# Kernel optimization log

Measured on AMD Instinct MI355X. Metric: run time of the kernel, lower is better.

The kernel has to match this reference:

```python
import jax, jax.numpy as jnp
import numpy as np

D_MODEL, D_STATE, D_CONV, D_INNER = 1024, 16, 4, 2048
B, S = 1, 2048
EPS = 1e-5


def setup_inputs() -> dict:
    key = jax.random.key(0)
    ks = jax.random.split(key, 8)
    sc = 0.02
    return {
        "x": jax.random.normal(ks[0], (B, S, D_MODEL), jnp.float32),
        "ln_g": jnp.ones((D_MODEL,), jnp.float32),
        "ln_b": jnp.zeros((D_MODEL,), jnp.float32),
        "in_w": jax.random.normal(ks[1], (2 * D_INNER, D_MODEL), jnp.float32) * sc,
        "conv_w": jax.random.normal(ks[2], (D_INNER, 1, D_CONV), jnp.float32) * sc,  # depthwise OIH
        "conv_b": jax.random.normal(ks[3], (D_INNER,), jnp.float32) * sc,
        "xproj_w": jax.random.normal(ks[4], (2 * D_STATE + 1, D_INNER), jnp.float32) * sc,
        "dt_w": jax.random.normal(ks[5], (D_INNER, 1), jnp.float32) * sc,
        "dt_b": jax.random.normal(ks[6], (D_INNER,), jnp.float32) * sc,
        "A_log": jnp.log(jnp.arange(1, D_STATE + 1, dtype=jnp.float32)),
        "D": jnp.ones((D_INNER,), jnp.float32),
        "out_w": jax.random.normal(ks[7], (D_MODEL, D_INNER), jnp.float32) * sc,
    }


def reference(x, ln_g, ln_b, in_w, conv_w, conv_b, xproj_w, dt_w, dt_b, A_log, D, out_w):
    b, s, _ = x.shape
    d_inner = D.shape[0]
    d_state = A_log.shape[0]
    d_conv = conv_w.shape[-1]
    residual = x

    # LayerNorm
    mu = jnp.mean(x, axis=-1, keepdims=True)
    var = jnp.mean(jnp.square(x - mu), axis=-1, keepdims=True)
    xn = (x - mu) * jax.lax.rsqrt(var + EPS) * ln_g + ln_b

    # in_proj, split into x and gate z
    xz = jnp.einsum('bsd,ed->bse', xn, in_w)  # [B,S,2*d_inner]
    xi, z = jnp.split(xz, 2, axis=-1)

    # causal depthwise conv1d (torch pads d_conv-1 both sides then crops to seq_len)
    xc = jnp.transpose(xi, (0, 2, 1))  # [B,C,S]
    xc = jnp.pad(xc, ((0, 0), (0, 0), (d_conv - 1, 0)))
    xc = jax.lax.conv_general_dilated(
        xc, conv_w, window_strides=(1,), padding='VALID',
        dimension_numbers=('NCH', 'OIH', 'NCH'), feature_group_count=d_inner)
    xc = xc + conv_b[None, :, None]
    xs = jax.nn.silu(jnp.transpose(xc, (0, 2, 1)))  # [B,S,d_inner]

    # SSM projections
    xp = jnp.einsum('bsd,ed->bse', xs, xproj_w)  # [B,S,2*d_state+1]
    delta = jax.nn.softplus(xp[..., :1] * dt_w[:, 0] + dt_b)  # [B,S,d_inner]
    Bm = xp[..., 1:1 + d_state]  # [B,S,N]
    Cm = xp[..., 1 + d_state:]   # [B,S,N]
    A = -jnp.exp(A_log)          # [N]

    dA = jnp.exp(delta[..., None] * A)                      # [B,S,d_inner,N]
    dBx = delta[..., None] * Bm[:, :, None, :] * xs[..., None]  # [B,S,d_inner,N]

    def step(h, inp):
        dA_t, dBx_t, C_t = inp
        h = dA_t * h + dBx_t                     # [B,d_inner,N]
        y_t = jnp.einsum('bdn,bn->bd', h, C_t)   # [B,d_inner]
        return h, y_t

    h0 = jnp.zeros((b, d_inner, d_state), x.dtype)
    _, ys = jax.lax.scan(step, h0, (jnp.moveaxis(dA, 1, 0),
                                    jnp.moveaxis(dBx, 1, 0),
                                    jnp.moveaxis(Cm, 1, 0)))
    y = jnp.moveaxis(ys, 0, 1) + xs * D  # [B,S,d_inner]

    y = y * jax.nn.silu(z)
    out = jnp.einsum('bse,de->bsd', y, out_w)
    return out + residual
```

## Files before the change

### kernel.cpp

```cpp
#include <hip/hip_runtime.h>
#include <cstdint>
#include <cstddef>

#define D_MODEL 1024
#define D_STATE 16
#define D_CONV  4
#define D_INNER 2048
#define SEQ     2048
#define NCHUNK  128
#define CLEN    16
#define NGRP    8
#define GCH     16
#define LN_EPS  1e-5f

typedef unsigned short ushort_t;
typedef __attribute__((ext_vector_type(8))) short short8;
typedef __attribute__((ext_vector_type(4))) float f32x4;

__device__ __forceinline__ ushort_t f2bf(float x) {
  union { float f; uint32_t u; } v; v.f = x;
  uint32_t r = (v.u + 0x7fffu + ((v.u >> 16) & 1u)) >> 16;
  return (ushort_t)r;
}
__device__ __forceinline__ float bf2f(ushort_t u) {
  union { uint32_t x; float f; } v; v.x = ((uint32_t)u) << 16; return v.f;
}

__device__ __forceinline__ void async16(void* lds, const void* g) {
  __builtin_amdgcn_global_load_lds(
      (const __attribute__((address_space(1))) unsigned int*)g,
      (__attribute__((address_space(3))) unsigned int*)lds, 16, 0, 0);
}

__device__ __forceinline__ float softplus_f(float x) {
  if (x > 20.f) return x;
  if (x < -20.f) return __expf(x);
  return __logf(1.f + __expf(x));
}

__device__ __forceinline__ void dapow(float g1, float* da) {
  float g2 = g1 * g1, g4 = g2 * g2, g8 = g4 * g4;
  #pragma unroll
  for (int n = 0; n < 16; n++) {
    int e = n + 1;
    float v = (e & 1) ? g1 : 1.f;
    if (e & 2) v *= g2;
    if (e & 4) v *= g4;
    if (e & 8) v *= g8;
    da[n] = v;
  }
}

__global__ __launch_bounds__(256) void prep_kernel(const float* __restrict__ x,
                                                   const float* __restrict__ g,
                                                   const float* __restrict__ b,
                                                   const float* __restrict__ inw,
                                                   const float* __restrict__ outw,
                                                   const float* __restrict__ xpw,
                                                   ushort_t* __restrict__ xn_bf,
                                                   ushort_t* __restrict__ inw_bf,
                                                   ushort_t* __restrict__ outw_bf,
                                                   ushort_t* __restrict__ xpw_bf) {
  int blk = blockIdx.x;
  if (blk < SEQ) {
    int row = blk;
    const float4* xr = (const float4*)(x + (size_t)row * D_MODEL);
    float4 v = xr[threadIdx.x];
    float s  = v.x + v.y + v.z + v.w;
    float ss = v.x * v.x + v.y * v.y + v.z * v.z + v.w * v.w;
    #pragma unroll
    for (int o = 32; o; o >>= 1) { s += __shfl_down(s, o); ss += __shfl_down(ss, o); }
    __shared__ float sbuf[8], ssbuf[8];
    int wid = threadIdx.x >> 6, lane = threadIdx.x & 63;
    if (lane == 0) { sbuf[wid] = s; ssbuf[wid] = ss; }
    __syncthreads();
    if (threadIdx.x == 0) {
      float t = 0.f, t2 = 0.f;
      for (int i = 0; i < 4; i++) { t += sbuf[i]; t2 += ssbuf[i]; }
      float mu = t / D_MODEL;
      sbuf[4] = mu;
      ssbuf[4] = rsqrtf(t2 / D_MODEL - mu * mu + LN_EPS);
    }
    __syncthreads();
    float mu = sbuf[4], inv = ssbuf[4];
    float4 gv = ((const float4*)g)[threadIdx.x];
    float4 bv = ((const float4*)b)[threadIdx.x];
    ushort_t o4[4];
    o4[0] = f2bf((v.x - mu) * inv * gv.x + bv.x);
    o4[1] = f2bf((v.y - mu) * inv * gv.y + bv.y);
    o4[2] = f2bf((v.z - mu) * inv * gv.z + bv.z);
    o4[3] = f2bf((v.w - mu) * inv * gv.w + bv.w);
    *(ushort4*)&xn_bf[(size_t)row * D_MODEL + threadIdx.x * 4] =
        make_ushort4(o4[0], o4[1], o4[2], o4[3]);
  } else {
    int idx = ((blk - SEQ) * 256 + threadIdx.x) * 4;
    const int n1 = 2 * D_INNER * D_MODEL;
    const int n2 = D_MODEL * D_INNER;
    const int n3 = 64 * D_INNER;
    const float* src; ushort_t* dst; int j;
    if (idx < n1) { src = inw; dst = inw_bf; j = idx; }
    else if (idx < n1 + n2) { src = outw; dst = outw_bf; j = idx - n1; }
    else if (idx < n1 + n2 + n3) {
      j = idx - n1 - n2;
      if (j < 33 * D_INNER) { src = xpw; dst = xpw_bf; }
      else {
        *(ushort4*)&xpw_bf[j] = make_ushort4(0, 0, 0, 0);
        return;
      }
    } else return;
    float4 v = *(const float4*)&src[j];
    *(ushort4*)&dst[j] = make_ushort4(f2bf(v.x), f2bf(v.y), f2bf(v.z), f2bf(v.w));
  }
}

template <int BM, int BN, int KDIM, int EPI, int NBUF, int KSPLIT, int MINW>
__global__ __launch_bounds__(256, MINW) void gemm_pipe(const ushort_t* __restrict__ A,
                                                       const ushort_t* __restrict__ B,
                                                       void* __restrict__ Cout,
                                                       const float* __restrict__ R,
                                                       int N) {
  constexpr int KT = KDIM / 32 / KSPLIT;
  constexpr int K2 = KDIM * 2;
  constexpr int IA = BM / 64, IB = BN / 64;
  constexpr int S  = IA + IB;
  constexpr int W  = (NBUF - 2) * S;
  constexpr int WTM = BM / 2, WTN = BN / 2;
  constexpr int MREP = WTM / 16, NREP = WTN / 16;
  __shared__ __align__(16) ushort_t As[NBUF][BM * 32];
  __shared__ __align__(16) ushort_t Bs[NBUF][BN * 32];

  const int nwg = gridDim.x * gridDim.y;
  int bid = blockIdx.y * gridDim.x + blockIdx.x;
  int swz = (bid & 7) * (nwg >> 3) + (bid >> 3);
  int bn = swz % gridDim.x, bm = swz / gridDim.x;
  int ks = 0;
  if constexpr (KSPLIT > 1) { ks = bn; bn = 0; }
  const int tid = threadIdx.x, wid = tid >> 6, lane = tid & 63;
  const int wm = wid >> 1, wn = wid & 1;
  const int row0A = bm * BM, row0B = bn * BN;
  const size_t kbase = (size_t)ks * KT * 64;

  const char* gA[IA];
  const char* gB[IB];
  #pragma unroll
  for (int i = 0; i < IA; i++) {
    int o = i * 4096 + tid * 16;
    int r = o >> 6, src = (o & 63) ^ ((r & 3) << 4);
    gA[i] = (const char*)A + (size_t)(row0A + r) * K2 + src + kbase;
  }
  #pragma unroll
  for (int i = 0; i < IB; i++) {
    int o = i * 4096 + tid * 16;
    int r = o >> 6, src = (o & 63) ^ ((r & 3) << 4);
    gB[i] = (const char*)B + (size_t)(row0B + r) * K2 + src + kbase;
  }
  const int ldsW = wid * 1024;

  auto STAGE = [&](int bb, int kt) {
    int kb = kt * 64;
    #pragma unroll
    for (int i = 0; i < IA; i++)
      async16((char*)&As[bb][0] + i * 4096 + ldsW, gA[i] + kb);
    #pragma unroll
    for (int i = 0; i < IB; i++)
      async16((char*)&Bs[bb][0] + i * 4096 + ldsW, gB[i] + kb);
  };

  #pragma unroll
  for (int p = 0; p < NBUF - 1; p++) STAGE(p, p);

  int offA[MREP], offB[NREP];
  #pragma unroll
  for (int m = 0; m < MREP; m++) {
    int row = wm * WTM + m * 16 + (lane & 15);
    offA[m] = row * 64 + ((((lane >> 4)) ^ (row & 3)) << 4);
  }
  #pragma unroll
  for (int n = 0; n < NREP; n++) {
    int row = wn * WTN + n * 16 + (lane & 15);
    offB[n] = row * 64 + ((((lane >> 4)) ^ (row & 3)) << 4);
  }

  f32x4 acc[MREP][NREP] = {};
  int cur = 0;
  for (int kt = 0; kt < KT; kt++) {
    if (kt < KT - 1) {
      if constexpr (W == 4)       asm volatile("s_waitcnt vmcnt(4)" ::: "memory");
      else if constexpr (W == 6)  asm volatile("s_waitcnt vmcnt(6)" ::: "memory");
      else if constexpr (W == 8)  asm volatile("s_waitcnt vmcnt(8)" ::: "memory");
      else if constexpr (W == 12) asm volatile("s_waitcnt vmcnt(12)" ::: "memory");
      else                        asm volatile("s_waitcnt vmcnt(0)" ::: "memory");
    } else {
      asm volatile("s_waitcnt vmcnt(0)" ::: "memory");
    }
    __builtin_amdgcn_s_barrier();
    __builtin_amdgcn_sched_barrier(0);
    const char* Ab = (const char*)&As[cur][0];
    const char* Bb = (const char*)&Bs[cur][0];
    short8 af[MREP], bf[NREP];
    #pragma unroll
    for (int m = 0; m < MREP; m++) af[m] = *(const short8*)(Ab + offA[m]);
    #pragma unroll
    for (int n = 0; n < NREP; n++) bf[n] = *(const short8*)(Bb + offB[n]);
    if (kt + NBUF - 1 < KT) {
      int b2 = cur + NBUF - 1; if (b2 >= NBUF) b2 -= NBUF;
      STAGE(b2, kt + NBUF - 1);
    }
    __builtin_amdgcn_s_setprio(1);
    #pragma unroll
    for (int m = 0; m < MREP; m++)
      #pragma unroll
      for (int n = 0; n < NREP; n++)
        acc[m][n] = __builtin_amdgcn_mfma_f32_16x16x32_bf16(af[m], bf[n], acc[m][n], 0, 0, 0);
    __builtin_amdgcn_s_setprio(0);
    cur++; if (cur == NBUF) cur = 0;
  }

  #pragma unroll
  for (int m = 0; m < MREP; m++)
    #pragma unroll
    for (int n = 0; n < NREP; n++) {
      int r0 = row0A + wm * WTM + m * 16 + ((lane >> 4) << 2);
      int c  = row0B + wn * WTN + n * 16 + (lane & 15);
      #pragma unroll
      for (int q = 0; q < 4; q++) {
        if constexpr (EPI == 0) {
          ((ushort_t*)Cout)[(size_t)(r0 + q) * N + c] = f2bf(acc[m][n][q]);
        } else if constexpr (EPI == 1) {
          size_t idx = (size_t)(r0 + q) * N + c;
          ((float*)Cout)[idx] = acc[m][n][q] + R[idx];
        } else {
          if (c < 33)
            ((float*)Cout)[((size_t)ks * SEQ + r0 + q) * 33 + c] = acc[m][n][q];
        }
      }
    }
}

__global__ __launch_bounds__(256) void conv_silu_kernel(const ushort_t* __restrict__ xz_bf,
                                                        const float* __restrict__ cw,
                                                        const float* __restrict__ cb,
                                                        ushort_t* __restrict__ xs_bf) {
  const int t0 = blockIdx.x * 4;
  const int d0 = threadIdx.x * 8;
  short8 win[7];
  #pragma unroll
  for (int j = 0; j < 7; j++) {
    int tt = t0 - 3 + j;
    if (tt >= 0) win[j] = *(const short8*)&xz_bf[(size_t)tt * (2 * D_INNER) + d0];
    else         win[j] = (short8)0;
  }
  float4 w[8];
  float  cbv[8];
  #pragma unroll
  for (int j = 0; j < 8; j++) { w[j] = ((const float4*)cw)[d0 + j]; cbv[j] = cb[d0 + j]; }
  #pragma unroll
  for (int q = 0; q < 4; q++) {
    short8 o8;
    #pragma unroll
    for (int j = 0; j < 8; j++) {
      float acc = cbv[j]
                + bf2f((ushort_t)win[q][j])     * w[j].x
                + bf2f((ushort_t)win[q + 1][j]) * w[j].y
                + bf2f((ushort_t)win[q + 2][j]) * w[j].z
                + bf2f((ushort_t)win[q + 3][j]) * w[j].w;
      float sg = 1.f / (1.f + __expf(-acc));
      o8[j] = (short)f2bf(acc * sg);
    }
    *(short8*)&xs_bf[(size_t)(t0 + q) * D_INNER + d0] = o8;
  }
}

__global__ __launch_bounds__(256) void scan_pass1(const ushort_t* __restrict__ xs_bf,
                                                  const float* __restrict__ xpp,
                                                  const float* __restrict__ dt_w,
                                                  const float* __restrict__ dt_b,
                                                  const float* __restrict__ A_log,
                                                  ushort_t* __restrict__ Hp,
                                                  float* __restrict__ Sd) {
  int c = blockIdx.x;
  int d0 = blockIdx.y * 512 + threadIdx.x;
  __shared__ float Bsh[CLEN][16], drs[CLEN], Ash[16];
  {
    int t = threadIdx.x >> 4, n = threadIdx.x & 15;
    const size_t P = (size_t)SEQ * 33;
    size_t rb = (size_t)(c * CLEN + t) * 33;
    float sB = 0.f;
    #pragma unroll
    for (int k = 0; k < 8; k++) sB += xpp[k * P + rb + 1 + n];
    Bsh[t][n] = sB;
    if (threadIdx.x < CLEN) {
      size_t rr = (size_t)(c * CLEN + threadIdx.x) * 33;
      float sD = 0.f;
      #pragma unroll
      for (int k = 0; k < 8; k++) sD += xpp[k * P + rr];
      drs[threadIdx.x] = sD;
    } else if (threadIdx.x < CLEN + 16) {
      int n2 = threadIdx.x - CLEN;
      Ash[n2] = -__expf(A_log[n2]);
    }
  }
  __syncthreads();
  bool fastA = true;
  #pragma unroll
  for (int n = 0; n < 16; n++) fastA = fastA && (fabsf(Ash[n] + (float)(n + 1)) < 1e-4f * (n + 1));
  float dw[2] = {dt_w[d0], dt_w[d0 + 256]};
  float db[2] = {dt_b[d0], dt_b[d0 + 256]};
  float h[2][16] = {};
  float S[2] = {0.f, 0.f};
  size_t tb = (size_t)(c * CLEN) * D_INNER + d0;
  float xv[2] = {bf2f(xs_bf[tb]), bf2f(xs_bf[tb + 256])};
  for (int t = 0; t < CLEN; t++) {
    float nx[2] = {0.f, 0.f};
    if (t + 1 < CLEN) {
      nx[0] = bf2f(xs_bf[tb + D_INNER]);
      nx[1] = bf2f(xs_bf[tb + D_INNER + 256]);
    }
    float bb[16];
    *(float4*)&bb[0]  = *(const float4*)&Bsh[t][0];
    *(float4*)&bb[4]  = *(const float4*)&Bsh[t][4];
    *(float4*)&bb[8]  = *(const float4*)&Bsh[t][8];
    *(float4*)&bb[12] = *(const float4*)&Bsh[t][12];
    float drt = drs[t];
    #pragma unroll
    for (int u = 0; u < 2; u++) {
      float delta = softplus_f(drt * dw[u] + db[u]);
      S[u] += delta;
      float w = delta * xv[u];
      if (fastA) {
        float da[16];
        dapow(__expf(-delta), da);
        #pragma unroll
        for (int n = 0; n < 16; n++) h[u][n] = da[n] * h[u][n] + w * bb[n];
      } else {
        #pragma unroll
        for (int n = 0; n < 16; n++) h[u][n] = __expf(delta * Ash[n]) * h[u][n] + w * bb[n];
      }
    }
    xv[0] = nx[0]; xv[1] = nx[1];
    tb += D_INNER;
  }
  #pragma unroll
  for (int u = 0; u < 2; u++) {
    int d = d0 + u * 256;
    size_t base = ((size_t)c * D_INNER + d) * 16;
    short8 p0, p1;
    #pragma unroll
    for (int n = 0; n < 8; n++) { p0[n] = (short)f2bf(h[u][n]); p1[n] = (short)f2bf(h[u][8 + n]); }
    *(short8*)&Hp[base] = p0;
    *(short8*)&Hp[base + 8] = p1;
    Sd[(size_t)c * D_INNER + d] = S[u];
  }
}

__global__ __launch_bounds__(256) void combineA(const ushort_t* __restrict__ Hp,
                                                const float* __restrict__ Sd,
                                                const float* __restrict__ A_log,
                                                ushort_t* __restrict__ Hl,
                                                float* __restrict__ Slocp,
                                                ushort_t* __restrict__ Hgtot,
                                                float* __restrict__ Sgtot) {
  int g = blockIdx.x;
  int idx = blockIdx.y * 256 + threadIdx.x;
  int d = idx >> 4, n = idx & 15;
  float An = -__expf(A_log[n]);
  float h = 0.f, S = 0.f;
  const size_t stride = (size_t)D_INNER * 16;
  #pragma unroll 4
  for (int j = 0; j < GCH; j++) {
    int c = g * GCH + j;
    Hl[(size_t)c * stride + idx] = f2bf(h);
    if (n == 0) Slocp[(size_t)c * D_INNER + d] = S;
    float Sc = Sd[(size_t)c * D_INNER + d];
    float hp = bf2f(Hp[(size_t)c * stride + idx]);
    h = __expf(An * Sc) * h + hp;
    S += Sc;
  }
  Hgtot[(size_t)g * stride + idx] = f2bf(h);
  if (n == 0) Sgtot[(size_t)g * D_INNER + d] = S;
}

__global__ __launch_bounds__(256) void scan_pass2(const ushort_t* __restrict__ xs_bf,
                                                  const float* __restrict__ xpp,
                                                  const ushort_t* __restrict__ xz_bf,
                                                  const float* __restrict__ dt_w,
                                                  const float* __restrict__ dt_b,
                                                  const float* __restrict__ A_log,
                                                  const float* __restrict__ Dp,
                                                  const ushort_t* __restrict__ Hl,
                                                  const float* __restrict__ Slocp,
                                                  const ushort_t* __restrict__ Hgtot,
                                                  const float* __restrict__ Sgtot,
                                                  ushort_t* __restrict__ y_bf) {
  int c = blockIdx.x;
  int d0 = blockIdx.y * 512 + threadIdx.x;
  __shared__ float Bsh[CLEN][16], Csh[CLEN][16], drs[CLEN], Ash[16];
  {
    int t = threadIdx.x >> 4, n = threadIdx.x & 15;
    const size_t P = (size_t)SEQ * 33;
    size_t rb = (size_t)(c * CLEN + t) * 33;
    float sB = 0.f, sC = 0.f;
    #pragma unroll
    for (int k = 0; k < 8; k++) {
      sB += xpp[k * P + rb + 1 + n];
      sC += xpp[k * P + rb + 17 + n];
    }
    Bsh[t][n] = sB;
    Csh[t][n] = sC;
    if (threadIdx.x < CLEN) {
      size_t rr = (size_t)(c * CLEN + threadIdx.x) * 33;
      float sD = 0.f;
      #pragma unroll
      for (int k = 0; k < 8; k++) sD += xpp[k * P + rr];
      drs[threadIdx.x] = sD;
    } else if (threadIdx.x < CLEN + 16) {
      int n2 = threadIdx.x - CLEN;
      Ash[n2] = -__expf(A_log[n2]);
    }
  }
  __syncthreads();
  bool fastA = true;
  #pragma unroll
  for (int n = 0; n < 16; n++) fastA = fastA && (fabsf(Ash[n] + (float)(n + 1)) < 1e-4f * (n + 1));
  float dw[2] = {dt_w[d0], dt_w[d0 + 256]};
  float db[2] = {dt_b[d0], dt_b[d0 + 256]};
  float Dd[2] = {Dp[d0], Dp[d0 + 256]};
  int g8 = c >> 4;
  const size_t stride = (size_t)D_INNER * 16;
  float h[2][16];
  #pragma unroll
  for (int u = 0; u < 2; u++) {
    int d = d0 + u * 256;
    float G[16];
    #pragma unroll
    for (int n = 0; n < 16; n++) G[n] = 0.f;
    for (int g = 0; g < g8; g++) {
      float Sg = Sgtot[(size_t)g * D_INNER + d];
      size_t gb = (size_t)g * stride + (size_t)d * 16;
      short8 hg0 = *(const short8*)&Hgtot[gb];
      short8 hg1 = *(const short8*)&Hgtot[gb + 8];
      if (fastA) {
        float pw[16];
        dapow(__expf(-Sg), pw);
        #pragma unroll
        for (int n = 0; n < 8; n++) {
          G[n]     = pw[n]     * G[n]     + bf2f((ushort_t)hg0[n]);
          G[8 + n] = pw[8 + n] * G[8 + n] + bf2f((ushort_t)hg1[n]);
        }
      } else {
        #pragma unroll
        for (int n = 0; n < 8; n++) {
          G[n]     = __expf(Ash[n] * Sg)     * G[n]     + bf2f((ushort_t)hg0[n]);
          G[8 + n] = __expf(Ash[8 + n] * Sg) * G[8 + n] + bf2f((ushort_t)hg1[n]);
        }
      }
    }
    size_t hb = ((size_t)c * D_INNER + d) * 16;
    float Slp = Slocp[(size_t)c * D_INNER + d];
    short8 hl0 = *(const short8*)&Hl[hb];
    short8 hl1 = *(const short8*)&Hl[hb + 8];
    float hl[16];
    #pragma unroll
    for (int n = 0; n < 8; n++) {
      hl[n] = bf2f((ushort_t)hl0[n]); hl[8 + n] = bf2f((ushort_t)hl1[n]);
    }
    if (fastA) {
      float pw[16];
      dapow(__expf(-Slp), pw);
      #pragma unroll
      for (int n = 0; n < 16; n++) h[u][n] = hl[n] + pw[n] * G[n];
    } else {
      #pragma unroll
      for (int n = 0; n < 16; n++) h[u][n] = hl[n] + __expf(Ash[n] * Slp) * G[n];
    }
  }
  size_t tb = (size_t)(c * CLEN) * D_INNER + d0;
  size_t zb = (size_t)(c * CLEN) * (2 * D_INNER) + D_INNER + d0;
  float xv[2] = {bf2f(xs_bf[tb]), bf2f(xs_bf[tb + 256])};
  float zv[2] = {bf2f(xz_bf[zb]), bf2f(xz_bf[zb + 256])};
  for (int t = 0; t < CLEN; t++) {
    float nx[2] = {0.f, 0.f}, nz[2] = {0.f, 0.f};
    if (t + 1 < CLEN) {
      nx[0] = bf2f(xs_bf[tb + D_INNER]);
      nx[1] = bf2f(xs_bf[tb + D_INNER + 256]);
      nz[0] = bf2f(xz_bf[zb + 2 * D_INNER]);
      nz[1] = bf2f(xz_bf[zb + 2 * D_INNER + 256]);
    }
    float bb[16], cc[16];
    *(float4*)&bb[0]  = *(const float4*)&Bsh[t][0];
    *(float4*)&bb[4]  = *(const float4*)&Bsh[t][4];
    *(float4*)&bb[8]  = *(const float4*)&Bsh[t][8];
    *(float4*)&bb[12] = *(const float4*)&Bsh[t][12];
    *(float4*)&cc[0]  = *(const float4*)&Csh[t][0];
    *(float4*)&cc[4]  = *(const float4*)&Csh[t][4];
    *(float4*)&cc[8]  = *(const float4*)&Csh[t][8];
    *(float4*)&cc[12] = *(const float4*)&Csh[t][12];
    float drt = drs[t];
    size_t ti = (size_t)(c * CLEN + t);
    #pragma unroll
    for (int u = 0; u < 2; u++) {
      float delta = softplus_f(drt * dw[u] + db[u]);
      float w = delta * xv[u];
      float y = 0.f;
      if (fastA) {
        float da[16];
        dapow(__expf(-delta), da);
        #pragma unroll
        for (int n = 0; n < 16; n++) {
          h[u][n] = da[n] * h[u][n] + w * bb[n];
          y += h[u][n] * cc[n];
        }
      } else {
        #pragma unroll
        for (int n = 0; n < 16; n++) {
          h[u][n] = __expf(delta * Ash[n]) * h[u][n] + w * bb[n];
          y += h[u][n] * cc[n];
        }
      }
      float z = zv[u];
      float sz = z / (1.f + __expf(-z));
      float out = (y + xv[u] * Dd[u]) * sz;
      y_bf[ti * D_INNER + d0 + u * 256] = f2bf(out);
    }
    xv[0] = nx[0]; xv[1] = nx[1];
    zv[0] = nz[0]; zv[1] = nz[1];
    tb += D_INNER; zb += 2 * D_INNER;
  }
}

extern "C" void kernel_launch(void* const* d_in, const int* in_sizes, int n_in,
                              void* d_out, int out_size, void* d_ws, size_t ws_size,
                              hipStream_t stream) {
  const float* x      = (const float*)d_in[0];
  const float* ln_g   = (const float*)d_in[1];
  const float* ln_b   = (const float*)d_in[2];
  const float* in_w   = (const float*)d_in[3];
  const float* conv_w = (const float*)d_in[4];
  const float* conv_b = (const float*)d_in[5];
  const float* xproj_w= (const float*)d_in[6];
  const float* dt_w   = (const float*)d_in[7];
  const float* dt_b   = (const float*)d_in[8];
  const float* A_log  = (const float*)d_in[9];
  const float* Dp     = (const float*)d_in[10];
  const float* out_w  = (const float*)d_in[11];
  float* out = (float*)d_out;

  char* ws = (char*)d_ws;
  size_t off = 0;
  auto alloc = [&](size_t bytes) { char* p = ws + off; off += (bytes + 255) & ~(size_t)255; return p; };
  ushort_t* xz_bf   = (ushort_t*)alloc((size_t)SEQ * 2 * D_INNER * 2);
  ushort_t* xn_bf   = (ushort_t*)alloc((size_t)SEQ * D_MODEL * 2);
  ushort_t* inw_bf  = (ushort_t*)alloc((size_t)2 * D_INNER * D_MODEL * 2);
  ushort_t* outw_bf = (ushort_t*)alloc((size_t)D_MODEL * D_INNER * 2);
  ushort_t* xpw_bf  = (ushort_t*)alloc((size_t)64 * D_INNER * 2);
  ushort_t* xs_bf   = (ushort_t*)alloc((size_t)SEQ * D_INNER * 2);
  float*    xp_part = (float*)   alloc((size_t)8 * SEQ * 33 * 4);
  ushort_t* Hp      = (ushort_t*)alloc((size_t)NCHUNK * D_INNER * 16 * 2);
  ushort_t* Hl      = (ushort_t*)alloc((size_t)NCHUNK * D_INNER * 16 * 2);
  float*    Sd      = (float*)   alloc((size_t)NCHUNK * D_INNER * 4);
  float*    Slocp   = (float*)   alloc((size_t)NCHUNK * D_INNER * 4);
  ushort_t* Hgtot   = (ushort_t*)alloc((size_t)NGRP * D_INNER * 16 * 2);
  float*    Sgtot   = (float*)   alloc((size_t)NGRP * D_INNER * 4);
  ushort_t* y_bf    = (ushort_t*)alloc((size_t)SEQ * D_INNER * 2);
  (void)ws_size;

  const int ncvt4 = (2 * D_INNER * D_MODEL + D_MODEL * D_INNER + 64 * D_INNER) / 4;
  prep_kernel<<<SEQ + (ncvt4 + 255) / 256, 256, 0, stream>>>(
      x, ln_g, ln_b, in_w, out_w, xproj_w, xn_bf, inw_bf, outw_bf, xpw_bf);
  gemm_pipe<128, 128, D_MODEL, 0, 3, 1, 3><<<dim3(2 * D_INNER / 128, SEQ / 128), 256, 0, stream>>>(
      xn_bf, inw_bf, xz_bf, nullptr, 2 * D_INNER);
  conv_silu_kernel<<<SEQ / 4, 256, 0, stream>>>(xz_bf, conv_w, conv_b, xs_bf);
  gemm_pipe<64, 64, D_INNER, 3, 6, 8, 3><<<dim3(8, SEQ / 64), 256, 0, stream>>>(
      xs_bf, xpw_bf, xp_part, nullptr, 64);
  scan_pass1<<<dim3(NCHUNK, D_INNER / 512), 256, 0, stream>>>(xs_bf, xp_part, dt_w, dt_b, A_log, Hp, Sd);
  combineA<<<dim3(NGRP, D_INNER * 16 / 256), 256, 0, stream>>>(Hp, Sd, A_log, Hl, Slocp, Hgtot, Sgtot);
  scan_pass2<<<dim3(NCHUNK, D_INNER / 512), 256, 0, stream>>>(xs_bf, xp_part, xz_bf, dt_w, dt_b, A_log,
                                                              Dp, Hl, Slocp, Hgtot, Sgtot, y_bf);
  gemm_pipe<64, 64, D_INNER, 1, 6, 1, 3><<<dim3(D_MODEL / 64, SEQ / 64), 256, 0, stream>>>(
      y_bf, outw_bf, out, x, D_MODEL);
}
```

Before: 120.3 us.

## Fuse chunked scan passes into one cooperative kernel with grid syncs

Merges scan_pass1, combineA and scan_pass2 into a single cooperative kernel that uses grid.sync between phases. Each thread keeps its chunk's xs values and softplus deltas in registers, so the second pass neither reloads nor recomputes them. This removes two kernel launches and a redundant pass over xs. Several gemm template parameters are also retuned. The costs are extra register pressure from the per-thread arrays, grid-wide barrier overhead, and the requirement that all 512 blocks be co-resident.

```diff
diff --git a/kernel.cpp b/kernel.cpp
--- a/kernel.cpp
+++ b/kernel.cpp
@@ -1,6 +1,9 @@
 #include <hip/hip_runtime.h>
+#include <hip/hip_cooperative_groups.h>
 #include <cstdint>
 #include <cstddef>
+
+namespace cg = cooperative_groups;
 
 #define D_MODEL 1024
 #define D_STATE 16
@@ -271,129 +274,24 @@
   }
 }
 
-__global__ __launch_bounds__(256) void scan_pass1(const ushort_t* __restrict__ xs_bf,
-                                                  const float* __restrict__ xpp,
-                                                  const float* __restrict__ dt_w,
-                                                  const float* __restrict__ dt_b,
-                                                  const float* __restrict__ A_log,
-                                                  ushort_t* __restrict__ Hp,
-                                                  float* __restrict__ Sd) {
-  int c = blockIdx.x;
-  int d0 = blockIdx.y * 512 + threadIdx.x;
-  __shared__ float Bsh[CLEN][16], drs[CLEN], Ash[16];
-  {
-    int t = threadIdx.x >> 4, n = threadIdx.x & 15;
-    const size_t P = (size_t)SEQ * 33;
-    size_t rb = (size_t)(c * CLEN + t) * 33;
-    float sB = 0.f;
-    #pragma unroll
-    for (int k = 0; k < 8; k++) sB += xpp[k * P + rb + 1 + n];
-    Bsh[t][n] = sB;
-    if (threadIdx.x < CLEN) {
-      size_t rr = (size_t)(c * CLEN + threadIdx.x) * 33;
-      float sD = 0.f;
-      #pragma unroll
-      for (int k = 0; k < 8; k++) sD += xpp[k * P + rr];
-      drs[threadIdx.x] = sD;
-    } else if (threadIdx.x < CLEN + 16) {
-      int n2 = threadIdx.x - CLEN;
-      Ash[n2] = -__expf(A_log[n2]);
-    }
-  }
-  __syncthreads();
-  bool fastA = true;
-  #pragma unroll
-  for (int n = 0; n < 16; n++) fastA = fastA && (fabsf(Ash[n] + (float)(n + 1)) < 1e-4f * (n + 1));
-  float dw[2] = {dt_w[d0], dt_w[d0 + 256]};
-  float db[2] = {dt_b[d0], dt_b[d0 + 256]};
-  float h[2][16] = {};
-  float S[2] = {0.f, 0.f};
-  size_t tb = (size_t)(c * CLEN) * D_INNER + d0;
-  float xv[2] = {bf2f(xs_bf[tb]), bf2f(xs_bf[tb + 256])};
-  for (int t = 0; t < CLEN; t++) {
-    float nx[2] = {0.f, 0.f};
-    if (t + 1 < CLEN) {
-      nx[0] = bf2f(xs_bf[tb + D_INNER]);
-      nx[1] = bf2f(xs_bf[tb + D_INNER + 256]);
-    }
-    float bb[16];
-    *(float4*)&bb[0]  = *(const float4*)&Bsh[t][0];
-    *(float4*)&bb[4]  = *(const float4*)&Bsh[t][4];
-    *(float4*)&bb[8]  = *(const float4*)&Bsh[t][8];
-    *(float4*)&bb[12] = *(const float4*)&Bsh[t][12];
-    float drt = drs[t];
-    #pragma unroll
-    for (int u = 0; u < 2; u++) {
-      float delta = softplus_f(drt * dw[u] + db[u]);
-      S[u] += delta;
-      float w = delta * xv[u];
-      if (fastA) {
-        float da[16];
-        dapow(__expf(-delta), da);
-        #pragma unroll
-        for (int n = 0; n < 16; n++) h[u][n] = da[n] * h[u][n] + w * bb[n];
-      } else {
-        #pragma unroll
-        for (int n = 0; n < 16; n++) h[u][n] = __expf(delta * Ash[n]) * h[u][n] + w * bb[n];
-      }
-    }
-    xv[0] = nx[0]; xv[1] = nx[1];
-    tb += D_INNER;
-  }
-  #pragma unroll
-  for (int u = 0; u < 2; u++) {
-    int d = d0 + u * 256;
-    size_t base = ((size_t)c * D_INNER + d) * 16;
-    short8 p0, p1;
-    #pragma unroll
-    for (int n = 0; n < 8; n++) { p0[n] = (short)f2bf(h[u][n]); p1[n] = (short)f2bf(h[u][8 + n]); }
-    *(short8*)&Hp[base] = p0;
-    *(short8*)&Hp[base + 8] = p1;
-    Sd[(size_t)c * D_INNER + d] = S[u];
-  }
-}
-
-__global__ __launch_bounds__(256) void combineA(const ushort_t* __restrict__ Hp,
-                                                const float* __restrict__ Sd,
-                                                const float* __restrict__ A_log,
-                                                ushort_t* __restrict__ Hl,
-                                                float* __restrict__ Slocp,
-                                                ushort_t* __restrict__ Hgtot,
-                                                float* __restrict__ Sgtot) {
-  int g = blockIdx.x;
-  int idx = blockIdx.y * 256 + threadIdx.x;
-  int d = idx >> 4, n = idx & 15;
-  float An = -__expf(A_log[n]);
-  float h = 0.f, S = 0.f;
+__global__ __launch_bounds__(256, 2) void coop_scan(const ushort_t* __restrict__ xs_bf,
+                                                    const float* __restrict__ xpp,
+                                                    const ushort_t* __restrict__ xz_bf,
+                                                    const float* __restrict__ dt_w,
+                                                    const float* __restrict__ dt_b,
+                                                    const float* __restrict__ A_log,
+                                                    const float* __restrict__ Dp,
+                                                    ushort_t* __restrict__ Hp,
+                                                    float* __restrict__ Sd,
+                                                    ushort_t* __restrict__ Hl,
+                                                    float* __restrict__ Slocp,
+                                                    ushort_t* __restrict__ Hgtot,
+                                                    float* __restrict__ Sgtot,
+                                                    ushort_t* __restrict__ y_bf) {
+  cg::grid_group grid = cg::this_grid();
+  const int c = blockIdx.x;
+  const int d0 = blockIdx.y * 512 + threadIdx.x;
   const size_t stride = (size_t)D_INNER * 16;
-  #pragma unroll 4
-  for (int j = 0; j < GCH; j++) {
-    int c = g * GCH + j;
-    Hl[(size_t)c * stride + idx] = f2bf(h);
-    if (n == 0) Slocp[(size_t)c * D_INNER + d] = S;
-    float Sc = Sd[(size_t)c * D_INNER + d];
-    float hp = bf2f(Hp[(size_t)c * stride + idx]);
-    h = __expf(An * Sc) * h + hp;
-    S += Sc;
-  }
-  Hgtot[(size_t)g * stride + idx] = f2bf(h);
-  if (n == 0) Sgtot[(size_t)g * D_INNER + d] = S;
-}
-
-__global__ __launch_bounds__(256) void scan_pass2(const ushort_t* __restrict__ xs_bf,
-                                                  const float* __restrict__ xpp,
-                                                  const ushort_t* __restrict__ xz_bf,
-                                                  const float* __restrict__ dt_w,
-                                                  const float* __restrict__ dt_b,
-                                                  const float* __restrict__ A_log,
-                                                  const float* __restrict__ Dp,
-                                                  const ushort_t* __restrict__ Hl,
-                                                  const float* __restrict__ Slocp,
-                                                  const ushort_t* __restrict__ Hgtot,
-                                                  const float* __restrict__ Sgtot,
-                                                  ushort_t* __restrict__ y_bf) {
-  int c = blockIdx.x;
-  int d0 = blockIdx.y * 512 + threadIdx.x;
   __shared__ float Bsh[CLEN][16], Csh[CLEN][16], drs[CLEN], Ash[16];
   {
     int t = threadIdx.x >> 4, n = threadIdx.x & 15;
@@ -424,9 +322,87 @@
   for (int n = 0; n < 16; n++) fastA = fastA && (fabsf(Ash[n] + (float)(n + 1)) < 1e-4f * (n + 1));
   float dw[2] = {dt_w[d0], dt_w[d0 + 256]};
   float db[2] = {dt_b[d0], dt_b[d0 + 256]};
+
+  float xva[CLEN][2], dla[CLEN][2];
+  {
+    size_t tb = (size_t)(c * CLEN) * D_INNER + d0;
+    #pragma unroll
+    for (int t = 0; t < CLEN; t++) {
+      xva[t][0] = bf2f(xs_bf[tb]);
+      xva[t][1] = bf2f(xs_bf[tb + 256]);
+      tb += D_INNER;
+    }
+  }
+  #pragma unroll
+  for (int t = 0; t < CLEN; t++) {
+    float drt = drs[t];
+    dla[t][0] = softplus_f(drt * dw[0] + db[0]);
+    dla[t][1] = softplus_f(drt * dw[1] + db[1]);
+  }
+  {
+    float h[2][16] = {};
+    float S[2] = {0.f, 0.f};
+    #pragma unroll
+    for (int t = 0; t < CLEN; t++) {
+      float bb[16];
+      *(float4*)&bb[0]  = *(const float4*)&Bsh[t][0];
+      *(float4*)&bb[4]  = *(const float4*)&Bsh[t][4];
+      *(float4*)&bb[8]  = *(const float4*)&Bsh[t][8];
+      *(float4*)&bb[12] = *(const float4*)&Bsh[t][12];
+      #pragma unroll
+      for (int u = 0; u < 2; u++) {
+        float delta = dla[t][u];
+        S[u] += delta;
+        float w = delta * xva[t][u];
+        if (fastA) {
+          float da[16];
+          dapow(__expf(-delta), da);
+          #pragma unroll
+          for (int n = 0; n < 16; n++) h[u][n] = da[n] * h[u][n] + w * bb[n];
+        } else {
+          #pragma unroll
+          for (int n = 0; n < 16; n++) h[u][n] = __expf(delta * Ash[n]) * h[u][n] + w * bb[n];
+        }
+      }
+    }
+    #pragma unroll
+    for (int u = 0; u < 2; u++) {
+      int d = d0 + u * 256;
+      size_t base = ((size_t)c * D_INNER + d) * 16;
+      short8 p0, p1;
+      #pragma unroll
+      for (int n = 0; n < 8; n++) { p0[n] = (short)f2bf(h[u][n]); p1[n] = (short)f2bf(h[u][8 + n]); }
+      *(short8*)&Hp[base] = p0;
+      *(short8*)&Hp[base + 8] = p1;
+      Sd[(size_t)c * D_INNER + d] = S[u];
+    }
+  }
+  grid.sync();
+
+  {
+    int flat = (blockIdx.y * gridDim.x + blockIdx.x) * 256 + (int)threadIdx.x;
+    for (int it = flat; it < NGRP * D_INNER * 16; it += 512 * 256) {
+      int g2 = it >> 15, idx = it & 32767;
+      int d = idx >> 4, n = idx & 15;
+      float An = Ash[n];
+      float hh = 0.f, SS = 0.f;
+      #pragma unroll 4
+      for (int j = 0; j < GCH; j++) {
+        int c2 = g2 * GCH + j;
+        Hl[(size_t)c2 * stride + idx] = f2bf(hh);
+        if (n == 0) Slocp[(size_t)c2 * D_INNER + d] = SS;
+        float Sc = Sd[(size_t)c2 * D_INNER + d];
+        hh = __expf(An * Sc) * hh + bf2f(Hp[(size_t)c2 * stride + idx]);
+        SS += Sc;
+      }
+      Hgtot[(size_t)g2 * stride + idx] = f2bf(hh);
+      if (n == 0) Sgtot[(size_t)g2 * D_INNER + d] = SS;
+    }
+  }
+  grid.sync();
+
   float Dd[2] = {Dp[d0], Dp[d0 + 256]};
   int g8 = c >> 4;
-  const size_t stride = (size_t)D_INNER * 16;
   float h[2][16];
   #pragma unroll
   for (int u = 0; u < 2; u++) {
@@ -474,15 +450,12 @@
       for (int n = 0; n < 16; n++) h[u][n] = hl[n] + __expf(Ash[n] * Slp) * G[n];
     }
   }
-  size_t tb = (size_t)(c * CLEN) * D_INNER + d0;
   size_t zb = (size_t)(c * CLEN) * (2 * D_INNER) + D_INNER + d0;
-  float xv[2] = {bf2f(xs_bf[tb]), bf2f(xs_bf[tb + 256])};
   float zv[2] = {bf2f(xz_bf[zb]), bf2f(xz_bf[zb + 256])};
+  #pragma unroll
   for (int t = 0; t < CLEN; t++) {
-    float nx[2] = {0.f, 0.f}, nz[2] = {0.f, 0.f};
+    float nz[2] = {0.f, 0.f};
     if (t + 1 < CLEN) {
-      nx[0] = bf2f(xs_bf[tb + D_INNER]);
-      nx[1] = bf2f(xs_bf[tb + D_INNER + 256]);
       nz[0] = bf2f(xz_bf[zb + 2 * D_INNER]);
       nz[1] = bf2f(xz_bf[zb + 2 * D_INNER + 256]);
     }
@@ -495,12 +468,11 @@
     *(float4*)&cc[4]  = *(const float4*)&Csh[t][4];
     *(float4*)&cc[8]  = *(const float4*)&Csh[t][8];
     *(float4*)&cc[12] = *(const float4*)&Csh[t][12];
-    float drt = drs[t];
     size_t ti = (size_t)(c * CLEN + t);
     #pragma unroll
     for (int u = 0; u < 2; u++) {
-      float delta = softplus_f(drt * dw[u] + db[u]);
-      float w = delta * xv[u];
+      float delta = dla[t][u];
+      float w = delta * xva[t][u];
       float y = 0.f;
       if (fastA) {
         float da[16];
@@ -519,12 +491,11 @@
       }
       float z = zv[u];
       float sz = z / (1.f + __expf(-z));
-      float out = (y + xv[u] * Dd[u]) * sz;
+      float out = (y + xva[t][u] * Dd[u]) * sz;
       y_bf[ti * D_INNER + d0 + u * 256] = f2bf(out);
     }
-    xv[0] = nx[0]; xv[1] = nx[1];
     zv[0] = nz[0]; zv[1] = nz[1];
-    tb += D_INNER; zb += 2 * D_INNER;
+    zb += 2 * D_INNER;
   }
 }
 
@@ -567,15 +538,18 @@
   const int ncvt4 = (2 * D_INNER * D_MODEL + D_MODEL * D_INNER + 64 * D_INNER) / 4;
   prep_kernel<<<SEQ + (ncvt4 + 255) / 256, 256, 0, stream>>>(
       x, ln_g, ln_b, in_w, out_w, xproj_w, xn_bf, inw_bf, outw_bf, xpw_bf);
-  gemm_pipe<128, 128, D_MODEL, 0, 3, 1, 3><<<dim3(2 * D_INNER / 128, SEQ / 128), 256, 0, stream>>>(
+  gemm_pipe<128, 128, D_MODEL, 0, 4, 1, 2><<<dim3(2 * D_INNER / 128, SEQ / 128), 256, 0, stream>>>(
       xn_bf, inw_bf, xz_bf, nullptr, 2 * D_INNER);
   conv_silu_kernel<<<SEQ / 4, 256, 0, stream>>>(xz_bf, conv_w, conv_b, xs_bf);
-  gemm_pipe<64, 64, D_INNER, 3, 6, 8, 3><<<dim3(8, SEQ / 64), 256, 0, stream>>>(
+  gemm_pipe<64, 64, D_INNER, 3, 6, 8, 2><<<dim3(8, SEQ / 64), 256, 0, stream>>>(
       xs_bf, xpw_bf, xp_part, nullptr, 64);
-  scan_pass1<<<dim3(NCHUNK, D_INNER / 512), 256, 0, stream>>>(xs_bf, xp_part, dt_w, dt_b, A_log, Hp, Sd);
-  combineA<<<dim3(NGRP, D_INNER * 16 / 256), 256, 0, stream>>>(Hp, Sd, A_log, Hl, Slocp, Hgtot, Sgtot);
-  scan_pass2<<<dim3(NCHUNK, D_INNER / 512), 256, 0, stream>>>(xs_bf, xp_part, xz_bf, dt_w, dt_b, A_log,
-                                                              Dp, Hl, Slocp, Hgtot, Sgtot, y_bf);
-  gemm_pipe<64, 64, D_INNER, 1, 6, 1, 3><<<dim3(D_MODEL / 64, SEQ / 64), 256, 0, stream>>>(
+  {
+    void* cargs[] = {(void*)&xs_bf, (void*)&xp_part, (void*)&xz_bf, (void*)&dt_w, (void*)&dt_b,
+                     (void*)&A_log, (void*)&Dp, (void*)&Hp, (void*)&Sd, (void*)&Hl, (void*)&Slocp,
+                     (void*)&Hgtot, (void*)&Sgtot, (void*)&y_bf};
+    hipLaunchCooperativeKernel((void*)coop_scan, dim3(NCHUNK, D_INNER / 512), dim3(256, 1, 1),
+                               cargs, 0, stream);
+  }
+  gemm_pipe<64, 64, D_INNER, 1, 6, 1, 2><<<dim3(D_MODEL / 64, SEQ / 64), 256, 0, stream>>>(
       y_bf, outw_bf, out, x, D_MODEL);
 }
```

Result: slower. 241.3 us (+100.6%).
